# Performance work log

Measured on AMD Instinct MI355X. Metric: run time of the kernel, lower is better.

## Reference

```python
import jax, jax.numpy as jnp
import numpy as np

B, N, C = 16, 2048, 512
EPS = 1e-9        # numerical_stabilizer
BN_EPS = 1e-5     # flax BatchNorm default epsilon


def setup_inputs() -> dict:
    key = jax.random.key(0)
    ks = jax.random.split(key, 9)
    s = 1.0 / np.sqrt(C)

    def w(k):
        return jax.random.normal(k, (C, C), jnp.float32) * s

    return {
        "x": jax.random.normal(ks[0], (B, N, C), jnp.float32),
        "Wq": w(ks[1]), "bq": jnp.zeros((C,), jnp.float32),
        "Wk": w(ks[2]), "bk": jnp.zeros((C,), jnp.float32),
        "Wv": w(ks[3]), "bv": jnp.zeros((C,), jnp.float32),
        "Wo": w(ks[4]), "bo": jnp.zeros((C,), jnp.float32),
        "bn_scale": jnp.ones((C,), jnp.float32),
        "bn_bias": jnp.zeros((C,), jnp.float32),
        "bn_mean": jnp.zeros((C,), jnp.float32),
        "bn_var": jnp.ones((C,), jnp.float32),
    }


def reference(x, Wq, bq, Wk, bk, Wv, bv, Wo, bo,
              bn_scale, bn_bias, bn_mean, bn_var):
    # 1x1 'Conv' projections == pointwise linear layers
    q = x @ Wq + bq                                   # [B,N,C]
    k = x @ Wk + bk
    v = x @ Wv + bv

    # attention scores + row softmax
    att = jax.nn.softmax(jnp.einsum('bmc,bnc->bmn', q, k), axis=-1)  # [B,M,N]

    # post-softmax column renormalization: A / (eps + sum_M A),
    # then einsum '...MN,...NC->...NC' contracts M, so the effective
    # per-point scale is colsum / (eps + colsum).
    col = jnp.sum(att, axis=1)                        # [B,N]
    scale = col / (EPS + col)                         # [B,N]
    out = scale[..., None] * v                        # [B,N,C]

    # attention_type == 'naive': no offset
    y = out @ Wo + bo
    # BatchNorm with running stats (train=False)
    y = (y - bn_mean) * jax.lax.rsqrt(bn_var + BN_EPS) * bn_scale + bn_bias
    return jax.nn.relu(y) + x
```

## Files before the change

### kernel.cpp

```cpp
#include <hip/hip_runtime.h>
#include <math.h>

#define BB 16
#define NN 2048
#define CC 512
#define MM (BB * NN)
#define NSPLIT 4

typedef _Float16 half8 __attribute__((ext_vector_type(8)));
typedef _Float16 half4 __attribute__((ext_vector_type(4)));
typedef float floatx4 __attribute__((ext_vector_type(4)));

#define GLD16(gp, lp) __builtin_amdgcn_global_load_lds( \
    (const __attribute__((address_space(1))) void*)(gp), \
    (__attribute__((address_space(3))) void*)(lp), 16, 0, 0)

__device__ __forceinline__ int foff(int row16base, int fr, int g4) {
    return (row16base + fr) * 32 + ((g4 ^ ((fr >> 1) & 3)) << 3);
}

__global__ __launch_bounds__(256)
void split_x(const float* __restrict__ x, _Float16* __restrict__ xh,
             _Float16* __restrict__ xl)
{
    const size_t i = ((size_t)blockIdx.x * 256 + threadIdx.x) * 4;
    const float4 v = *(const float4*)(x + i);
    half4 h, l;
    h[0] = (_Float16)v.x; l[0] = (_Float16)(v.x - (float)h[0]);
    h[1] = (_Float16)v.y; l[1] = (_Float16)(v.y - (float)h[1]);
    h[2] = (_Float16)v.z; l[2] = (_Float16)(v.z - (float)h[2]);
    h[3] = (_Float16)v.w; l[3] = (_Float16)(v.w - (float)h[3]);
    *(half4*)(xh + i) = h;
    *(half4*)(xl + i) = l;
}

__global__ __launch_bounds__(256)
void conv_wT(const float* __restrict__ W, _Float16* __restrict__ Wt)
{
    const int o = blockIdx.x * 256 + threadIdx.x;
    const int n = o >> 9, k = o & 511;
    Wt[o] = (_Float16)W[k * 512 + n];
}

__global__ __launch_bounds__(256)
void calc_w2(const float* __restrict__ Wk, const float* __restrict__ bq,
             float* __restrict__ w2)
{
    const int i = blockIdx.x * 256 + threadIdx.x;
    if (i < 512) {
        float s = 0.0f;
        for (int j = 0; j < 512; ++j) s += Wk[i * 512 + j] * bq[j];
        w2[i] = s;
    }
}

__global__ __launch_bounds__(256)
void calc_beta(const float* __restrict__ x, const float* __restrict__ w2,
               float* __restrict__ bet)
{
    const int w = threadIdx.x >> 6, lane = threadIdx.x & 63;
    const int m = blockIdx.x * 4 + w;
    const float* xr = x + (size_t)m * CC;
    float s = 0.0f;
    for (int c = lane; c < CC; c += 64) s += xr[c] * w2[c];
    for (int off = 1; off < 64; off <<= 1) s += __shfl_xor(s, off);
    if (lane == 0) bet[m] = s;
}

__global__ __launch_bounds__(256)
void gemm_nt_split(const float* __restrict__ A, const float* __restrict__ Bm,
                   _Float16* __restrict__ outh, _Float16* __restrict__ outl)
{
    __shared__ float As[16][64];
    __shared__ float Bs[16][64];
    const int t = threadIdx.x, tc = t & 15, tr = t >> 4;
    const int j0 = blockIdx.x * 64, i0 = blockIdx.y * 64;
    const int lm = t >> 2, lk4 = (t & 3) << 2;
    float acc[4][4] = {};
    for (int kt = 0; kt < 512; kt += 16) {
        const float4 xa = *(const float4*)(A + (size_t)(j0 + lm) * 512 + kt + lk4);
        As[lk4 + 0][lm] = xa.x; As[lk4 + 1][lm] = xa.y;
        As[lk4 + 2][lm] = xa.z; As[lk4 + 3][lm] = xa.w;
        const float4 xb = *(const float4*)(Bm + (size_t)(i0 + lm) * 512 + kt + lk4);
        Bs[lk4 + 0][lm] = xb.x; Bs[lk4 + 1][lm] = xb.y;
        Bs[lk4 + 2][lm] = xb.z; Bs[lk4 + 3][lm] = xb.w;
        __syncthreads();
#pragma unroll
        for (int k = 0; k < 16; ++k) {
            float av[4], bv[4];
            *(float4*)av = *(const float4*)&As[k][tr * 4];
            *(float4*)bv = *(const float4*)&Bs[k][tc * 4];
#pragma unroll
            for (int i = 0; i < 4; ++i)
#pragma unroll
                for (int j = 0; j < 4; ++j)
                    acc[i][j] = fmaf(av[i], bv[j], acc[i][j]);
        }
        __syncthreads();
    }
#pragma unroll
    for (int i = 0; i < 4; ++i) {
        const int row = j0 + tr * 4 + i;
#pragma unroll
        for (int j = 0; j < 4; ++j) {
            const int col = i0 + tc * 4 + j;
            const float y = acc[i][j];
            const _Float16 h = (_Float16)y;
            outh[row * 512 + col] = h;
            outl[row * 512 + col] = (_Float16)(y - (float)h);
        }
    }
}

template<bool SPLIT, int MODE>
__global__ __launch_bounds__(256, 2)
void gemm16(const _Float16* __restrict__ Ah, const _Float16* __restrict__ Al,
            const _Float16* __restrict__ Bh, const _Float16* __restrict__ Bl,
            const float* __restrict__ bias, const float* __restrict__ colsc,
            const float* __restrict__ bn_scale, const float* __restrict__ bn_bias,
            const float* __restrict__ bn_mean, const float* __restrict__ bn_var,
            const float* __restrict__ xres,
            _Float16* __restrict__ oh, _Float16* __restrict__ ol,
            float* __restrict__ outf)
{
    __shared__ __align__(16) _Float16 sA0[128 * 32], sA1[128 * 32], sA2[128 * 32];
    __shared__ __align__(16) _Float16 sB0[256 * 32], sB1[256 * 32], sB2[256 * 32];

    const int t = threadIdx.x, lane = t & 63, w = t >> 6;
    const int m0 = blockIdx.x * 128, n0 = blockIdx.y * 256;
    const int lr4 = lane >> 2;
    const int sw8 = (((lane & 3) ^ ((lr4 >> 1) & 3)) << 3);
    const int fr = lane & 15, g4 = lane >> 4;
    const int wr = (w >> 1) * 64, wc = (w & 1) * 128;

    floatx4 acc[4][8];
#pragma unroll
    for (int i = 0; i < 4; ++i)
#pragma unroll
        for (int j = 0; j < 8; ++j) acc[i][j] = (floatx4){0.f, 0.f, 0.f, 0.f};

    auto stage = [&](_Float16* Sa, _Float16* Sb, int gt) {
        const int kt = gt * 32;
#pragma unroll
        for (int c = 0; c < 2; ++c) {
            const int r = w * 32 + c * 16;
            GLD16(Ah + (size_t)(m0 + r + lr4) * CC + kt + sw8, Sa + r * 32);
        }
#pragma unroll
        for (int c = 0; c < 4; ++c) {
            const int r = w * 64 + c * 16;
            GLD16(Bh + (size_t)(n0 + r + lr4) * CC + kt + sw8, Sb + r * 32);
        }
    };

    auto tile = [&](const _Float16* Ra, const _Float16* Rb,
                    _Float16* Sa, _Float16* Sb, int gt, int mode) {
        const int kt = gt * 32;
        half8 fal[4], fbl[8];
        if constexpr (SPLIT) {
#pragma unroll
            for (int rt = 0; rt < 4; ++rt)
                fal[rt] = *(const half8*)(Al + (size_t)(m0 + wr + rt * 16 + fr) * CC
                                          + kt + g4 * 8);
#pragma unroll
            for (int ct = 0; ct < 8; ++ct)
                fbl[ct] = *(const half8*)(Bl + (size_t)(n0 + wc + ct * 16 + fr) * CC
                                          + kt + g4 * 8);
        }
        if (mode == 0) stage(Sa, Sb, gt + 2);
        half8 fa[4];
#pragma unroll
        for (int rt = 0; rt < 4; ++rt)
            fa[rt] = *(const half8*)&Ra[foff(wr + rt * 16, fr, g4)];
#pragma unroll
        for (int hh = 0; hh < 2; ++hh) {
            half8 fb[4];
#pragma unroll
            for (int c4 = 0; c4 < 4; ++c4)
                fb[c4] = *(const half8*)&Rb[foff(wc + (hh * 4 + c4) * 16, fr, g4)];
            __builtin_amdgcn_s_setprio(1);
#pragma unroll
            for (int rt = 0; rt < 4; ++rt)
#pragma unroll
                for (int c4 = 0; c4 < 4; ++c4) {
                    const int ct = hh * 4 + c4;
                    acc[rt][ct] = __builtin_amdgcn_mfma_f32_16x16x32_f16(
                        fa[rt], fb[c4], acc[rt][ct], 0, 0, 0);
                    if constexpr (SPLIT) {
                        acc[rt][ct] = __builtin_amdgcn_mfma_f32_16x16x32_f16(
                            fa[rt], fbl[ct], acc[rt][ct], 0, 0, 0);
                        acc[rt][ct] = __builtin_amdgcn_mfma_f32_16x16x32_f16(
                            fal[rt], fb[c4], acc[rt][ct], 0, 0, 0);
                    }
                }
            __builtin_amdgcn_s_setprio(0);
        }
        if (mode == 0)      asm volatile("s_waitcnt vmcnt(6)" ::: "memory");
        else if (mode == 1) asm volatile("s_waitcnt vmcnt(0)" ::: "memory");
        __builtin_amdgcn_s_barrier();
        asm volatile("" ::: "memory");
    };

    stage(sA0, sB0, 0);
    stage(sA1, sB1, 1);
    asm volatile("s_waitcnt vmcnt(6)" ::: "memory");
    __builtin_amdgcn_s_barrier();
    asm volatile("" ::: "memory");

#pragma unroll 1
    for (int u = 0; u < 4; ++u) {
        const int gt = u * 3;
        tile(sA0, sB0, sA2, sB2, gt,     0);
        tile(sA1, sB1, sA0, sB0, gt + 1, 0);
        tile(sA2, sB2, sA1, sB1, gt + 2, 0);
    }
    tile(sA0, sB0, sA2, sB2, 12, 0);
    tile(sA1, sB1, sA0, sB0, 13, 0);
    tile(sA2, sB2, nullptr, nullptr, 14, 1);
    tile(sA0, sB0, nullptr, nullptr, 15, 2);

#pragma unroll
    for (int rt = 0; rt < 4; ++rt)
#pragma unroll
        for (int ct = 0; ct < 8; ++ct) {
            const int col = n0 + wc + ct * 16 + fr;
#pragma unroll
            for (int reg = 0; reg < 4; ++reg) {
                const int row = m0 + wr + rt * 16 + g4 * 4 + reg;
                float y = acc[rt][ct][reg];
                if constexpr (MODE == 0) {
                    const _Float16 h = (_Float16)y;
                    oh[(size_t)row * CC + col] = h;
                    ol[(size_t)row * CC + col] = (_Float16)(y - (float)h);
                } else if constexpr (MODE == 1) {
                    y = (y + bias[col]) * colsc[row];
                    oh[(size_t)row * CC + col] = (_Float16)y;
                } else {
                    y += bias[col];
                    y = (y - bn_mean[col]) * rsqrtf(bn_var[col] + 1e-5f)
                            * bn_scale[col] + bn_bias[col];
                    y = fmaxf(y, 0.0f) + xres[(size_t)row * CC + col];
                    outf[(size_t)row * CC + col] = y;
                }
            }
        }
}

__device__ __forceinline__ void attn_decode3(int& xt, int& b, int& sp) {
    const int h = blockIdx.x + (blockIdx.y << 4) + (blockIdx.z << 8);
    xt = (h >> 3) & 15;
    const int g = ((h >> 7) << 3) | (h & 7);
    b = g & 15;
    sp = g >> 4;
}
__device__ __forceinline__ void attn_decode_col(int& xt, int& b, int& sp) {
    const int h = blockIdx.x + (blockIdx.y << 3) + (blockIdx.z << 7);
    xt = (h >> 3) & 7;
    const int g = ((h >> 6) << 3) | (h & 7);
    b = g & 15;
    sp = g >> 4;
}

__global__ __launch_bounds__(256, 2)
void attn_rowstats(const _Float16* __restrict__ ah_, const _Float16* __restrict__ al_,
                   const _Float16* __restrict__ xh_,
                   const float* __restrict__ bet,
                   float* __restrict__ pm, float* __restrict__ pl)
{
    __shared__ __align__(16) _Float16 A0[128 * 32], A1[128 * 32], A2[128 * 32];
    __shared__ __align__(16) _Float16 X0[256 * 32], X1[256 * 32], X2[256 * 32];
    __shared__ float wm[4][64], wl[4][64];

    int xt, b, sp;
    attn_decode3(xt, b, sp);
    const int m0 = xt * 128;
    const int t = threadIdx.x, lane = t & 63, w = t >> 6;
    const int lr4 = lane >> 2;
    const int sw8 = (((lane & 3) ^ ((lr4 >> 1) & 3)) << 3);
    const int fr = lane & 15, g4 = lane >> 4;
    const int wr = (w >> 1) * 64, wc = (w & 1) * 128;
    const size_t bbase = (size_t)b * NN;

    float betA[8], betB[8];
#pragma unroll
    for (int ct = 0; ct < 8; ++ct) {
        betA[ct] = bet[bbase + sp * 512 +   0 + wc + ct * 16 + fr];
        betB[ct] = bet[bbase + sp * 512 + 256 + wc + ct * 16 + fr];
    }

    float m_st[4][4], l_st[4][4];
#pragma unroll
    for (int i = 0; i < 4; ++i)
#pragma unroll
        for (int j = 0; j < 4; ++j) { m_st[i][j] = -3.0e38f; l_st[i][j] = 0.0f; }

    floatx4 acc[4][8];
#pragma unroll
    for (int i = 0; i < 4; ++i)
#pragma unroll
        for (int j = 0; j < 8; ++j) acc[i][j] = (floatx4){0.f, 0.f, 0.f, 0.f};

    auto stage = [&](_Float16* Sa, _Float16* Sx, int gt) {
        const int nn0 = sp * 512 + (gt >> 4) * 256;
        const int nkt = (gt & 15) * 32;
#pragma unroll
        for (int c = 0; c < 2; ++c) {
            const int r = w * 32 + c * 16;
            GLD16(ah_ + (bbase + m0 + r + lr4) * CC + nkt + sw8, Sa + r * 32);
        }
#pragma unroll
        for (int c = 0; c < 4; ++c) {
            const int r = w * 64 + c * 16;
            GLD16(xh_ + (bbase + nn0 + r + lr4) * CC + nkt + sw8, Sx + r * 32);
        }
    };

    auto tile = [&](const _Float16* Ra, const _Float16* Rx,
                    _Float16* Sa, _Float16* Sx, int gt, int mode) {
        const int kt = (gt & 15) * 32;
        half8 fal[4];
#pragma unroll
        for (int rt = 0; rt < 4; ++rt)
            fal[rt] = *(const half8*)(al_ + (bbase + m0 + wr + rt * 16 + fr) * CC
                                      + kt + g4 * 8);
        if (mode == 0) stage(Sa, Sx, gt + 2);
        half8 fa[4];
#pragma unroll
        for (int rt = 0; rt < 4; ++rt)
            fa[rt] = *(const half8*)&Ra[foff(wr + rt * 16, fr, g4)];
#pragma unroll
        for (int hh = 0; hh < 2; ++hh) {
            half8 fb[4];
#pragma unroll
            for (int c4 = 0; c4 < 4; ++c4)
                fb[c4] = *(const half8*)&Rx[foff(wc + (hh * 4 + c4) * 16, fr, g4)];
            __builtin_amdgcn_s_setprio(1);
#pragma unroll
            for (int rt = 0; rt < 4; ++rt)
#pragma unroll
                for (int c4 = 0; c4 < 4; ++c4) {
                    acc[rt][hh * 4 + c4] = __builtin_amdgcn_mfma_f32_16x16x32_f16(
                        fa[rt], fb[c4], acc[rt][hh * 4 + c4], 0, 0, 0);
                    acc[rt][hh * 4 + c4] = __builtin_amdgcn_mfma_f32_16x16x32_f16(
                        fal[rt], fb[c4], acc[rt][hh * 4 + c4], 0, 0, 0);
                }
            __builtin_amdgcn_s_setprio(0);
        }
        if ((gt & 15) == 15) {
            const bool c1 = (gt >> 4) != 0;
#pragma unroll
            for (int rt = 0; rt < 4; ++rt)
#pragma unroll
                for (int reg = 0; reg < 4; ++reg) {
                    float v[8];
#pragma unroll
                    for (int ct = 0; ct < 8; ++ct)
                        v[ct] = acc[rt][ct][reg] + (c1 ? betB[ct] : betA[ct]);
                    float mx = v[0];
#pragma unroll
                    for (int ct = 1; ct < 8; ++ct) mx = fmaxf(mx, v[ct]);
                    const float mo = m_st[rt][reg];
                    const float mn = fmaxf(mo, mx);
                    float s = 0.0f;
#pragma unroll
                    for (int ct = 0; ct < 8; ++ct) s += __expf(v[ct] - mn);
                    l_st[rt][reg] = l_st[rt][reg] * __expf(mo - mn) + s;
                    m_st[rt][reg] = mn;
                }
#pragma unroll
            for (int i = 0; i < 4; ++i)
#pragma unroll
                for (int j = 0; j < 8; ++j) acc[i][j] = (floatx4){0.f, 0.f, 0.f, 0.f};
        }
        if (mode == 0)      asm volatile("s_waitcnt vmcnt(6)" ::: "memory");
        else if (mode == 1) asm volatile("s_waitcnt vmcnt(0)" ::: "memory");
        __builtin_amdgcn_s_barrier();
        asm volatile("" ::: "memory");
    };

    stage(A0, X0, 0);
    stage(A1, X1, 1);
    asm volatile("s_waitcnt vmcnt(6)" ::: "memory");
    __builtin_amdgcn_s_barrier();
    asm volatile("" ::: "memory");

#pragma unroll 1
    for (int u = 0; u < 10; ++u) {
        const int gt = u * 3;
        tile(A0, X0, A2, X2, gt,     0);
        tile(A1, X1, A0, X0, gt + 1, 0);
        tile(A2, X2, A1, X1, gt + 2, 0);
    }
    tile(A0, X0, nullptr, nullptr, 30, 1);
    tile(A1, X1, nullptr, nullptr, 31, 2);

#pragma unroll
    for (int rt = 0; rt < 4; ++rt)
#pragma unroll
        for (int reg = 0; reg < 4; ++reg) {
            float m = m_st[rt][reg], l = l_st[rt][reg];
#pragma unroll
            for (int off = 1; off < 16; off <<= 1) {
                const float mo = __shfl_xor(m, off);
                const float lo = __shfl_xor(l, off);
                const float mn = fmaxf(m, mo);
                l = l * __expf(m - mn) + lo * __expf(mo - mn);
                m = mn;
            }
            if (fr == 0) {
                wm[w][rt * 16 + g4 * 4 + reg] = m;
                wl[w][rt * 16 + g4 * 4 + reg] = l;
            }
        }
    __syncthreads();
    if (t < 128) {
        const int r = t & 63;
        const int wa = (t < 64) ? 0 : 2, wb = wa + 1;
        const float ma = wm[wa][r], mb = wm[wb][r];
        const float M = fmaxf(ma, mb);
        const float L = wl[wa][r] * __expf(ma - M) + wl[wb][r] * __expf(mb - M);
        pm[(size_t)sp * MM + bbase + m0 + t] = M;
        pl[(size_t)sp * MM + bbase + m0 + t] = L;
    }
}

__global__ __launch_bounds__(256)
void rho_merge(const float* __restrict__ pm, const float* __restrict__ pl,
               float* __restrict__ rho)
{
    const size_t i = (size_t)blockIdx.x * 256 + threadIdx.x;
    float M = pm[i];
#pragma unroll
    for (int s = 1; s < NSPLIT; ++s) M = fmaxf(M, pm[s * (size_t)MM + i]);
    float L = 0.0f;
#pragma unroll
    for (int s = 0; s < NSPLIT; ++s)
        L += pl[s * (size_t)MM + i] * __expf(pm[s * (size_t)MM + i] - M);
    rho[i] = M + __logf(L);
}

__global__ __launch_bounds__(256, 2)
void attn_colsum(const _Float16* __restrict__ ah_, const _Float16* __restrict__ al_,
                 const _Float16* __restrict__ xh_,
                 const float* __restrict__ bet, const float* __restrict__ rho,
                 float* __restrict__ pc)
{
    __shared__ __align__(16) _Float16 A0[128 * 32], A1[128 * 32], A2[128 * 32];
    __shared__ __align__(16) _Float16 X0[256 * 32], X1[256 * 32], X2[256 * 32];
    __shared__ float cred[4][128];

    int xt, b, sp;
    attn_decode_col(xt, b, sp);
    const int n0 = xt * 256;
    const int t = threadIdx.x, lane = t & 63, w = t >> 6;
    const int lr4 = lane >> 2;
    const int sw8 = (((lane & 3) ^ ((lr4 >> 1) & 3)) << 3);
    const int fr = lane & 15, g4 = lane >> 4;
    const int wr = (w >> 1) * 64, wc = (w & 1) * 128;
    const size_t bbase = (size_t)b * NN;

    float bet_r[8];
#pragma unroll
    for (int ct = 0; ct < 8; ++ct)
        bet_r[ct] = bet[bbase + n0 + wc + ct * 16 + fr];

    float csum[8] = {0.f, 0.f, 0.f, 0.f, 0.f, 0.f, 0.f, 0.f};
    floatx4 rr[4];
    floatx4 acc[4][8];
#pragma unroll
    for (int i = 0; i < 4; ++i)
#pragma unroll
        for (int j = 0; j < 8; ++j) acc[i][j] = (floatx4){0.f, 0.f, 0.f, 0.f};

    auto stage = [&](_Float16* Sa, _Float16* Sx, int gt) {
        const int nm0 = sp * 512 + (gt >> 4) * 128;
        const int nkt = (gt & 15) * 32;
#pragma unroll
        for (int c = 0; c < 2; ++c) {
            const int r = w * 32 + c * 16;
            GLD16(ah_ + (bbase + nm0 + r + lr4) * CC + nkt + sw8, Sa + r * 32);
        }
#pragma unroll
        for (int c = 0; c < 4; ++c) {
            const int r = w * 64 + c * 16;
            GLD16(xh_ + (bbase + n0 + r + lr4) * CC + nkt + sw8, Sx + r * 32);
        }
    };

    auto tile = [&](const _Float16* Ra, const _Float16* Rx,
                    _Float16* Sa, _Float16* Sx, int gt, int mode) {
        const int kt = (gt & 15) * 32;
        const int m0c = sp * 512 + (gt >> 4) * 128;
        if ((gt & 15) == 0) {
#pragma unroll
            for (int rt = 0; rt < 4; ++rt)
                rr[rt] = *(const floatx4*)&rho[bbase + m0c + wr + rt * 16 + g4 * 4];
        }
        half8 fal[4];
#pragma unroll
        for (int rt = 0; rt < 4; ++rt)
            fal[rt] = *(const half8*)(al_ + (bbase + m0c + wr + rt * 16 + fr) * CC
                                      + kt + g4 * 8);
        if (mode == 0) stage(Sa, Sx, gt + 2);
        half8 fa[4];
#pragma unroll
        for (int rt = 0; rt < 4; ++rt)
            fa[rt] = *(const half8*)&Ra[foff(wr + rt * 16, fr, g4)];
#pragma unroll
        for (int hh = 0; hh < 2; ++hh) {
            half8 fb[4];
#pragma unroll
            for (int c4 = 0; c4 < 4; ++c4)
                fb[c4] = *(const half8*)&Rx[foff(wc + (hh * 4 + c4) * 16, fr, g4)];
            __builtin_amdgcn_s_setprio(1);
#pragma unroll
            for (int rt = 0; rt < 4; ++rt)
#pragma unroll
                for (int c4 = 0; c4 < 4; ++c4) {
                    acc[rt][hh * 4 + c4] = __builtin_amdgcn_mfma_f32_16x16x32_f16(
                        fa[rt], fb[c4], acc[rt][hh * 4 + c4], 0, 0, 0);
                    acc[rt][hh * 4 + c4] = __builtin_amdgcn_mfma_f32_16x16x32_f16(
                        fal[rt], fb[c4], acc[rt][hh * 4 + c4], 0, 0, 0);
                }
            __builtin_amdgcn_s_setprio(0);
        }
        if ((gt & 15) == 15) {
#pragma unroll
            for (int rt = 0; rt < 4; ++rt)
#pragma unroll
                for (int reg = 0; reg < 4; ++reg) {
                    const float r = rr[rt][reg];
#pragma unroll
                    for (int ct = 0; ct < 8; ++ct)
                        csum[ct] += __expf(acc[rt][ct][reg] + bet_r[ct] - r);
                }
#pragma unroll
            for (int i = 0; i < 4; ++i)
#pragma unroll
                for (int j = 0; j < 8; ++j) acc[i][j] = (floatx4){0.f, 0.f, 0.f, 0.f};
        }
        if (mode == 0)      asm volatile("s_waitcnt vmcnt(6)" ::: "memory");
        else if (mode == 1) asm volatile("s_waitcnt vmcnt(0)" ::: "memory");
        __builtin_amdgcn_s_barrier();
        asm volatile("" ::: "memory");
    };

    stage(A0, X0, 0);
    stage(A1, X1, 1);
    asm volatile("s_waitcnt vmcnt(6)" ::: "memory");
    __builtin_amdgcn_s_barrier();
    asm volatile("" ::: "memory");

#pragma unroll 1
    for (int u = 0; u < 20; ++u) {
        const int gt = u * 3;
        tile(A0, X0, A2, X2, gt,     0);
        tile(A1, X1, A0, X0, gt + 1, 0);
        tile(A2, X2, A1, X1, gt + 2, 0);
    }
    tile(A0, X0, A2, X2, 60, 0);
    tile(A1, X1, A0, X0, 61, 0);
    tile(A2, X2, nullptr, nullptr, 62, 1);
    tile(A0, X0, nullptr, nullptr, 63, 2);

#pragma unroll
    for (int ct = 0; ct < 8; ++ct) {
        csum[ct] += __shfl_xor(csum[ct], 16);
        csum[ct] += __shfl_xor(csum[ct], 32);
    }
    if (lane < 16)
#pragma unroll
        for (int ct = 0; ct < 8; ++ct) cred[w][ct * 16 + lane] = csum[ct];
    __syncthreads();
    if (t < 256) {
        const int c = t & 127;
        const float s = (t < 128) ? (cred[0][c] + cred[2][c])
                                  : (cred[1][c] + cred[3][c]);
        pc[(size_t)sp * MM + bbase + n0 + t] = s;
    }
}

__global__ __launch_bounds__(256)
void colsc_merge(const float* __restrict__ pc, float* __restrict__ colsc)
{
    const size_t i = (size_t)blockIdx.x * 256 + threadIdx.x;
    float c = 0.0f;
#pragma unroll
    for (int s = 0; s < NSPLIT; ++s) c += pc[s * (size_t)MM + i];
    colsc[i] = c / (1e-9f + c);
}

extern "C" void kernel_launch(void* const* d_in, const int* in_sizes, int n_in,
                              void* d_out, int out_size, void* d_ws, size_t ws_size,
                              hipStream_t stream)
{
    const float* x        = (const float*)d_in[0];
    const float* Wq       = (const float*)d_in[1];
    const float* bq       = (const float*)d_in[2];
    const float* Wk       = (const float*)d_in[3];
    const float* bk       = (const float*)d_in[4];   (void)bk;
    const float* Wv       = (const float*)d_in[5];
    const float* bv       = (const float*)d_in[6];
    const float* Wo       = (const float*)d_in[7];
    const float* bo       = (const float*)d_in[8];
    const float* bn_scale = (const float*)d_in[9];
    const float* bn_bias  = (const float*)d_in[10];
    const float* bn_mean  = (const float*)d_in[11];
    const float* bn_var   = (const float*)d_in[12];
    float* out = (float*)d_out;

    const size_t MMC = (size_t)MM * CC;
    _Float16* xh = (_Float16*)d_ws;
    _Float16* xl = xh + MMC;
    _Float16* ah = xl + MMC;
    _Float16* al = ah + MMC;
    _Float16* th  = al;
    _Float16* Wvt = ah;
    _Float16* Wot = ah + 512 * 512;

    char* ob = (char*)d_out;
    _Float16* Pth = (_Float16*)(ob);
    _Float16* Ptl = (_Float16*)(ob + (1u << 19));
    float* w2     = (float*)(ob + (2u << 19));
    float* bet    = (float*)(ob + (2u << 19) + 8192);
    float* rho    = (float*)(ob + 1318912);
    float* colsc  = (float*)(ob + 1449984);
    float* pm     = (float*)(ob + 1581056);
    float* pl     = (float*)(ob + 2105344);
    float* pc     = (float*)(ob + 2629632);

    const dim3 blk(256);
    const dim3 g16(MM / 128, CC / 256);
    const dim3 grow(NN / 128, BB, NSPLIT);
    const dim3 gcol(NN / 256, BB, NSPLIT);

    split_x<<<MMC / (256 * 4), blk, 0, stream>>>(x, xh, xl);
    gemm_nt_split<<<dim3(8, 8), blk, 0, stream>>>(Wk, Wq, Pth, Ptl);
    calc_w2<<<2, blk, 0, stream>>>(Wk, bq, w2);
    calc_beta<<<MM / 4, blk, 0, stream>>>(x, w2, bet);

    gemm16<true, 0><<<g16, blk, 0, stream>>>(xh, xl, Pth, Ptl,
        nullptr, nullptr, nullptr, nullptr, nullptr, nullptr, nullptr,
        ah, al, nullptr);

    attn_rowstats<<<grow, blk, 0, stream>>>(ah, al, xh, bet, pm, pl);
    rho_merge<<<MM / 256, blk, 0, stream>>>(pm, pl, rho);
    attn_colsum<<<gcol, blk, 0, stream>>>(ah, al, xh, bet, rho, pc);
    colsc_merge<<<MM / 256, blk, 0, stream>>>(pc, colsc);

    conv_wT<<<1024, blk, 0, stream>>>(Wv, Wvt);
    gemm16<false, 1><<<g16, blk, 0, stream>>>(xh, nullptr, Wvt, nullptr,
        bv, colsc, nullptr, nullptr, nullptr, nullptr, nullptr,
        th, nullptr, nullptr);

    conv_wT<<<1024, blk, 0, stream>>>(Wo, Wot);
    gemm16<false, 2><<<g16, blk, 0, stream>>>(th, nullptr, Wot, nullptr,
        bo, nullptr, bn_scale, bn_bias, bn_mean, bn_var, x,
        nullptr, nullptr, out);
}
```

Before: 671.7 us.

## Fuse beta into x split and add dedicated LDS-staged split-precision GEMM

Merges the separate calc_beta pass into the x fp16 hi/lo split kernel, so x is read once and one launch is dropped. The split-precision projection GEMM moves to a new kernel with a 128x128 tile that stages both the high and low fp16 parts through LDS. The old path loaded the low parts straight from global memory without LDS staging. The new kernel has no multi-buffer pipelining, since it syncs twice per k-step, which may expose load latency. The non-split GEMMs lose their template branches.

```diff
diff --git a/kernel.cpp b/kernel.cpp
--- a/kernel.cpp
+++ b/kernel.cpp
@@ -20,10 +20,25 @@
 }
 
 __global__ __launch_bounds__(256)
-void split_x(const float* __restrict__ x, _Float16* __restrict__ xh,
-             _Float16* __restrict__ xl)
-{
-    const size_t i = ((size_t)blockIdx.x * 256 + threadIdx.x) * 4;
+void calc_w2(const float* __restrict__ Wk, const float* __restrict__ bq,
+             float* __restrict__ w2)
+{
+    const int i = blockIdx.x * 256 + threadIdx.x;
+    if (i < 512) {
+        float s = 0.0f;
+        for (int j = 0; j < 512; ++j) s += Wk[i * 512 + j] * bq[j];
+        w2[i] = s;
+    }
+}
+
+__global__ __launch_bounds__(256)
+void split_x_beta(const float* __restrict__ x, const float* __restrict__ w2,
+                  _Float16* __restrict__ xh, _Float16* __restrict__ xl,
+                  float* __restrict__ bet)
+{
+    __shared__ float part[4];
+    const int t = threadIdx.x;
+    const size_t i = (size_t)blockIdx.x * 1024 + (size_t)t * 4;
     const float4 v = *(const float4*)(x + i);
     half4 h, l;
     h[0] = (_Float16)v.x; l[0] = (_Float16)(v.x - (float)h[0]);
@@ -32,6 +47,17 @@
     h[3] = (_Float16)v.w; l[3] = (_Float16)(v.w - (float)h[3]);
     *(half4*)(xh + i) = h;
     *(half4*)(xl + i) = l;
+
+    const float4 wv = *(const float4*)(w2 + ((t * 4) & 511));
+    float s = v.x * wv.x + v.y * wv.y + v.z * wv.z + v.w * wv.w;
+#pragma unroll
+    for (int off = 1; off < 64; off <<= 1) s += __shfl_xor(s, off);
+    const int w = t >> 6;
+    if ((t & 63) == 0) part[w] = s;
+    __syncthreads();
+    const int m0 = blockIdx.x * 2;
+    if (t == 0)   bet[m0]     = part[0] + part[1];
+    if (t == 128) bet[m0 + 1] = part[2] + part[3];
 }
 
 __global__ __launch_bounds__(256)
@@ -40,31 +66,6 @@
     const int o = blockIdx.x * 256 + threadIdx.x;
     const int n = o >> 9, k = o & 511;
     Wt[o] = (_Float16)W[k * 512 + n];
-}
-
-__global__ __launch_bounds__(256)
-void calc_w2(const float* __restrict__ Wk, const float* __restrict__ bq,
-             float* __restrict__ w2)
-{
-    const int i = blockIdx.x * 256 + threadIdx.x;
-    if (i < 512) {
-        float s = 0.0f;
-        for (int j = 0; j < 512; ++j) s += Wk[i * 512 + j] * bq[j];
-        w2[i] = s;
-    }
-}
-
-__global__ __launch_bounds__(256)
-void calc_beta(const float* __restrict__ x, const float* __restrict__ w2,
-               float* __restrict__ bet)
-{
-    const int w = threadIdx.x >> 6, lane = threadIdx.x & 63;
-    const int m = blockIdx.x * 4 + w;
-    const float* xr = x + (size_t)m * CC;
-    float s = 0.0f;
-    for (int c = lane; c < CC; c += 64) s += xr[c] * w2[c];
-    for (int off = 1; off < 64; off <<= 1) s += __shfl_xor(s, off);
-    if (lane == 0) bet[m] = s;
 }
 
 __global__ __launch_bounds__(256)
@@ -112,16 +113,89 @@
     }
 }
 
-template<bool SPLIT, int MODE>
+__global__ __launch_bounds__(256)
+void gemm16_split(const _Float16* __restrict__ Ah, const _Float16* __restrict__ Al,
+                  const _Float16* __restrict__ Bh, const _Float16* __restrict__ Bl,
+                  _Float16* __restrict__ oh, _Float16* __restrict__ ol)
+{
+    __shared__ __align__(16) _Float16 sAh[128 * 32], sBh[128 * 32];
+    __shared__ __align__(16) _Float16 sAl[128 * 32], sBl[128 * 32];
+
+    const int t = threadIdx.x, lane = t & 63, w = t >> 6;
+    const int m0 = blockIdx.x * 128, n0 = blockIdx.y * 128;
+    const int lr4 = lane >> 2;
+    const int sw8 = (((lane & 3) ^ ((lr4 >> 1) & 3)) << 3);
+    const int fr = lane & 15, g4 = lane >> 4;
+    const int wr = (w >> 1) * 64, wc = (w & 1) * 64;
+
+    floatx4 acc[4][4];
+#pragma unroll
+    for (int i = 0; i < 4; ++i)
+#pragma unroll
+        for (int j = 0; j < 4; ++j) acc[i][j] = (floatx4){0.f, 0.f, 0.f, 0.f};
+
+    for (int kt = 0; kt < CC; kt += 32) {
+#pragma unroll
+        for (int c = 0; c < 2; ++c) {
+            const int r = w * 32 + c * 16;
+            const size_t goA = (size_t)(m0 + r + lr4) * CC + kt + sw8;
+            const size_t goB = (size_t)(n0 + r + lr4) * CC + kt + sw8;
+            GLD16(Ah + goA, sAh + r * 32);
+            GLD16(Bh + goB, sBh + r * 32);
+            GLD16(Al + goA, sAl + r * 32);
+            GLD16(Bl + goB, sBl + r * 32);
+        }
+        __syncthreads();
+
+        half8 fa[4], fb[4], fal[4], fbl[4];
+#pragma unroll
+        for (int rt = 0; rt < 4; ++rt) {
+            fa[rt]  = *(const half8*)&sAh[foff(wr + rt * 16, fr, g4)];
+            fal[rt] = *(const half8*)&sAl[foff(wr + rt * 16, fr, g4)];
+        }
+#pragma unroll
+        for (int ct = 0; ct < 4; ++ct) {
+            fb[ct]  = *(const half8*)&sBh[foff(wc + ct * 16, fr, g4)];
+            fbl[ct] = *(const half8*)&sBl[foff(wc + ct * 16, fr, g4)];
+        }
+#pragma unroll
+        for (int rt = 0; rt < 4; ++rt)
+#pragma unroll
+            for (int ct = 0; ct < 4; ++ct) {
+                acc[rt][ct] = __builtin_amdgcn_mfma_f32_16x16x32_f16(
+                    fa[rt], fb[ct], acc[rt][ct], 0, 0, 0);
+                acc[rt][ct] = __builtin_amdgcn_mfma_f32_16x16x32_f16(
+                    fa[rt], fbl[ct], acc[rt][ct], 0, 0, 0);
+                acc[rt][ct] = __builtin_amdgcn_mfma_f32_16x16x32_f16(
+                    fal[rt], fb[ct], acc[rt][ct], 0, 0, 0);
+            }
+        __syncthreads();
+    }
+
+#pragma unroll
+    for (int rt = 0; rt < 4; ++rt)
+#pragma unroll
+        for (int ct = 0; ct < 4; ++ct) {
+            const int col = n0 + wc + ct * 16 + fr;
+#pragma unroll
+            for (int reg = 0; reg < 4; ++reg) {
+                const int row = m0 + wr + rt * 16 + g4 * 4 + reg;
+                const float y = acc[rt][ct][reg];
+                const _Float16 h = (_Float16)y;
+                oh[(size_t)row * CC + col] = h;
+                ol[(size_t)row * CC + col] = (_Float16)(y - (float)h);
+            }
+        }
+}
+
+template<int MODE>
 __global__ __launch_bounds__(256, 2)
-void gemm16(const _Float16* __restrict__ Ah, const _Float16* __restrict__ Al,
-            const _Float16* __restrict__ Bh, const _Float16* __restrict__ Bl,
-            const float* __restrict__ bias, const float* __restrict__ colsc,
-            const float* __restrict__ bn_scale, const float* __restrict__ bn_bias,
-            const float* __restrict__ bn_mean, const float* __restrict__ bn_var,
-            const float* __restrict__ xres,
-            _Float16* __restrict__ oh, _Float16* __restrict__ ol,
-            float* __restrict__ outf)
+void gemm16n(const _Float16* __restrict__ Ah, const _Float16* __restrict__ Bh,
+             const float* __restrict__ bias, const float* __restrict__ colsc,
+             const float* __restrict__ bn_scale, const float* __restrict__ bn_bias,
+             const float* __restrict__ bn_mean, const float* __restrict__ bn_var,
+             const float* __restrict__ xres,
+             _Float16* __restrict__ oh, float* __restrict__ outf)
 {
     __shared__ __align__(16) _Float16 sA0[128 * 32], sA1[128 * 32], sA2[128 * 32];
     __shared__ __align__(16) _Float16 sB0[256 * 32], sB1[256 * 32], sB2[256 * 32];
@@ -155,18 +229,6 @@
 
     auto tile = [&](const _Float16* Ra, const _Float16* Rb,
                     _Float16* Sa, _Float16* Sb, int gt, int mode) {
-        const int kt = gt * 32;
-        half8 fal[4], fbl[8];
-        if constexpr (SPLIT) {
-#pragma unroll
-            for (int rt = 0; rt < 4; ++rt)
-                fal[rt] = *(const half8*)(Al + (size_t)(m0 + wr + rt * 16 + fr) * CC
-                                          + kt + g4 * 8);
-#pragma unroll
-            for (int ct = 0; ct < 8; ++ct)
-                fbl[ct] = *(const half8*)(Bl + (size_t)(n0 + wc + ct * 16 + fr) * CC
-                                          + kt + g4 * 8);
-        }
         if (mode == 0) stage(Sa, Sb, gt + 2);
         half8 fa[4];
 #pragma unroll
@@ -182,17 +244,9 @@
 #pragma unroll
             for (int rt = 0; rt < 4; ++rt)
 #pragma unroll
-                for (int c4 = 0; c4 < 4; ++c4) {
-                    const int ct = hh * 4 + c4;
-                    acc[rt][ct] = __builtin_amdgcn_mfma_f32_16x16x32_f16(
-                        fa[rt], fb[c4], acc[rt][ct], 0, 0, 0);
-                    if constexpr (SPLIT) {
-                        acc[rt][ct] = __builtin_amdgcn_mfma_f32_16x16x32_f16(
-                            fa[rt], fbl[ct], acc[rt][ct], 0, 0, 0);
-                        acc[rt][ct] = __builtin_amdgcn_mfma_f32_16x16x32_f16(
-                            fal[rt], fb[c4], acc[rt][ct], 0, 0, 0);
-                    }
-                }
+                for (int c4 = 0; c4 < 4; ++c4)
+                    acc[rt][hh * 4 + c4] = __builtin_amdgcn_mfma_f32_16x16x32_f16(
+                        fa[rt], fb[c4], acc[rt][hh * 4 + c4], 0, 0, 0);
             __builtin_amdgcn_s_setprio(0);
         }
         if (mode == 0)      asm volatile("s_waitcnt vmcnt(6)" ::: "memory");
@@ -228,11 +282,7 @@
             for (int reg = 0; reg < 4; ++reg) {
                 const int row = m0 + wr + rt * 16 + g4 * 4 + reg;
                 float y = acc[rt][ct][reg];
-                if constexpr (MODE == 0) {
-                    const _Float16 h = (_Float16)y;
-                    oh[(size_t)row * CC + col] = h;
-                    ol[(size_t)row * CC + col] = (_Float16)(y - (float)h);
-                } else if constexpr (MODE == 1) {
+                if constexpr (MODE == 1) {
                     y = (y + bias[col]) * colsc[row];
                     oh[(size_t)row * CC + col] = (_Float16)y;
                 } else {
@@ -630,18 +680,16 @@
     float* pc     = (float*)(ob + 2629632);
 
     const dim3 blk(256);
-    const dim3 g16(MM / 128, CC / 256);
+    const dim3 ga(MM / 128, CC / 128);
+    const dim3 gn(MM / 128, CC / 256);
     const dim3 grow(NN / 128, BB, NSPLIT);
     const dim3 gcol(NN / 256, BB, NSPLIT);
 
-    split_x<<<MMC / (256 * 4), blk, 0, stream>>>(x, xh, xl);
+    calc_w2<<<2, blk, 0, stream>>>(Wk, bq, w2);
+    split_x_beta<<<MMC / 1024, blk, 0, stream>>>(x, w2, xh, xl, bet);
     gemm_nt_split<<<dim3(8, 8), blk, 0, stream>>>(Wk, Wq, Pth, Ptl);
-    calc_w2<<<2, blk, 0, stream>>>(Wk, bq, w2);
-    calc_beta<<<MM / 4, blk, 0, stream>>>(x, w2, bet);
-
-    gemm16<true, 0><<<g16, blk, 0, stream>>>(xh, xl, Pth, Ptl,
-        nullptr, nullptr, nullptr, nullptr, nullptr, nullptr, nullptr,
-        ah, al, nullptr);
+
+    gemm16_split<<<ga, blk, 0, stream>>>(xh, xl, Pth, Ptl, ah, al);
 
     attn_rowstats<<<grow, blk, 0, stream>>>(ah, al, xh, bet, pm, pl);
     rho_merge<<<MM / 256, blk, 0, stream>>>(pm, pl, rho);
@@ -649,12 +697,10 @@
     colsc_merge<<<MM / 256, blk, 0, stream>>>(pc, colsc);
 
     conv_wT<<<1024, blk, 0, stream>>>(Wv, Wvt);
-    gemm16<false, 1><<<g16, blk, 0, stream>>>(xh, nullptr, Wvt, nullptr,
-        bv, colsc, nullptr, nullptr, nullptr, nullptr, nullptr,
-        th, nullptr, nullptr);
+    gemm16n<1><<<gn, blk, 0, stream>>>(xh, Wvt, bv, colsc,
+        nullptr, nullptr, nullptr, nullptr, nullptr, th, nullptr);
 
     conv_wT<<<1024, blk, 0, stream>>>(Wo, Wot);
-    gemm16<false, 2><<<g16, blk, 0, stream>>>(th, nullptr, Wot, nullptr,
-        bo, nullptr, bn_scale, bn_bias, bn_mean, bn_var, x,
-        nullptr, nullptr, out);
-}
+    gemm16n<2><<<gn, blk, 0, stream>>>(th, Wot, bo, nullptr,
+        bn_scale, bn_bias, bn_mean, bn_var, x, nullptr, out);
+}
```

New measurement: 589.1 us. -12.3%, faster.
